# Performance work log

Hardware: AMD Instinct MI355X
Metric: run time of the kernel (lower is better)

The kernel has to match this reference:

```python
import jax, jax.numpy as jnp
import numpy as np

N_HEAD = 8
N_FEAT = 512
D_HEAD = N_FEAT // N_HEAD


def setup_inputs() -> dict:
    key = jax.random.key(0)
    ks = jax.random.split(key, 11)
    B, T, L = 4, 2048, 16
    s = 1.0 / np.sqrt(D_HEAD)
    so = 1.0 / np.sqrt(N_FEAT)
    return {
        "q": jax.random.normal(ks[0], (B, T, 1, N_FEAT), jnp.float32),
        "k": jax.random.normal(ks[1], (B, T, L, N_FEAT), jnp.float32),
        "v": jax.random.normal(ks[2], (B, T, L, N_FEAT), jnp.float32),
        "Wq": jax.random.uniform(ks[3], (D_HEAD, D_HEAD), jnp.float32, -s, s),
        "bq": jax.random.uniform(ks[4], (D_HEAD,), jnp.float32, -s, s),
        "Wk": jax.random.uniform(ks[5], (D_HEAD, D_HEAD), jnp.float32, -s, s),
        "bk": jax.random.uniform(ks[6], (D_HEAD,), jnp.float32, -s, s),
        "Wv": jax.random.uniform(ks[7], (D_HEAD, D_HEAD), jnp.float32, -s, s),
        "bv": jax.random.uniform(ks[8], (D_HEAD,), jnp.float32, -s, s),
        "Wo": jax.random.uniform(ks[9], (N_FEAT, N_FEAT), jnp.float32, -so, so),
        "bo": jax.random.uniform(ks[10], (N_FEAT,), jnp.float32, -so, so),
    }


def reference(q, k, v, Wq, bq, Wk, bk, Wv, bv, Wo, bo):
    B, T, L, F = k.shape
    H, D = N_HEAD, D_HEAD
    # split heads: q [B,T,H,D] (query axis of length 1 squeezed), k/v [B,T,L,H,D]
    qh = q.reshape(B, T, H, D)
    kh = k.reshape(B, T, L, H, D)
    vh = v.reshape(B, T, L, H, D)
    # per-head linear projections (shared across heads), Linear: x @ W^T + b
    qh = jnp.einsum("bthd,ed->bthe", qh, Wq) + bq
    kh = jnp.einsum("btlhd,ed->btlhe", kh, Wk) + bk
    vh = jnp.einsum("btlhd,ed->btlhe", vh, Wv) + bv
    # attention scores over the local window L (query length 1 per timestep)
    attw = jnp.einsum("bthd,btlhd->bthl", qh, kh) / jnp.sqrt(jnp.asarray(D, qh.dtype))
    attn = jax.nn.softmax(attw, axis=-1)  # dropout is identity in eval mode
    ct = jnp.einsum("bthl,btlhd->bthd", attn, vh)
    ct = ct.reshape(B, T, F)
    return ct @ Wo.T + bo
```

## Files before the change

### kernel.cpp

```cpp
#include <hip/hip_runtime.h>


#define NFEAT 512
#define NHEAD 8
#define DHEAD 64
#define LWIN  16
#define MPOS  16
#define LDSP  20

__device__ __forceinline__ float lanebcast(float x, int l) {
    return __uint_as_float(__builtin_amdgcn_readlane(__float_as_uint(x), l));
}

__global__ void precompute_small(const float* __restrict__ Wq, const float* __restrict__ bq,
                                 const float* __restrict__ Wk,
                                 const float* __restrict__ Wo, const float* __restrict__ bo,
                                 const float* __restrict__ bv,
                                 float* __restrict__ A, float* __restrict__ g,
                                 float* __restrict__ b2) {
    int idx = blockIdx.x * 256 + threadIdx.x;
    if (idx < 4096) {
        int d = idx >> 6, dp = idx & 63;
        float s = 0.f;
        #pragma unroll 8
        for (int e = 0; e < 64; ++e) s = fmaf(Wq[e * 64 + d], Wk[e * 64 + dp], s);
        A[idx] = s;
    } else if (idx < 4160) {
        int dp = idx - 4096;
        float s = 0.f;
        #pragma unroll 8
        for (int e = 0; e < 64; ++e) s = fmaf(Wk[e * 64 + dp], bq[e], s);
        g[dp] = s;
    } else if (idx < 4672) {
        int j = idx - 4160;
        float s = bo[j];
        #pragma unroll 8
        for (int i = 0; i < 512; ++i) s = fmaf(Wo[j * 512 + i], bv[i & 63], s);
        b2[j] = s;
    }
}

__global__ void precompute_wo2(const float* __restrict__ Wo, const float* __restrict__ Wv,
                               float* __restrict__ Wo2T) {
    int idx = blockIdx.x * 256 + threadIdx.x;
    int i = idx & 511, j = idx >> 9;
    int h = i >> 6, e = i & 63;
    float s = 0.f;
    #pragma unroll 8
    for (int d = 0; d < 64; ++d)
        s = fmaf(Wo[j * 512 + h * 64 + d], Wv[d * 64 + e], s);
    Wo2T[(size_t)i * 512 + j] = s;
}

__global__ __launch_bounds__(512, 4)
void attn_main(const float* __restrict__ q, const float* __restrict__ k,
               const float* __restrict__ v,
               const float* __restrict__ A, const float* __restrict__ g,
               const float* __restrict__ b2, const float* __restrict__ Wo2T,
               float* __restrict__ out) {
    __shared__ __align__(16) float vbarT[NFEAT * LDSP];

    const int tid  = threadIdx.x;
    const int lane = tid & 63;
    const int fe   = tid;
    const int bt0  = blockIdx.x * MPOS;

    float Areg[64];
    #pragma unroll
    for (int d = 0; d < 64; ++d) Areg[d] = A[d * 64 + lane];
    const float greg = g[lane];

    for (int p = 0; p < MPOS; ++p) {
        const int bt = bt0 + p;
        const float qv = q[(size_t)bt * NFEAT + fe];

        float w = greg;
        #pragma unroll
        for (int d = 0; d < 64; ++d)
            w = fmaf(lanebcast(qv, d), Areg[d], w);
        w *= 0.125f;

        const float* kp = k + (size_t)bt * (LWIN * NFEAT) + fe;
        float kv[LWIN];
        #pragma unroll
        for (int l = 0; l < LWIN; ++l) kv[l] = kp[(size_t)l * NFEAT];
        float sc[LWIN];
        #pragma unroll
        for (int l = 0; l < LWIN; ++l) sc[l] = w * kv[l];
        #pragma unroll
        for (int m = 1; m < 64; m <<= 1) {
            #pragma unroll
            for (int l = 0; l < LWIN; ++l) sc[l] += __shfl_xor(sc[l], m, 64);
        }

        float mx = sc[0];
        #pragma unroll
        for (int l = 1; l < LWIN; ++l) mx = fmaxf(mx, sc[l]);
        float sum = 0.f;
        #pragma unroll
        for (int l = 0; l < LWIN; ++l) { sc[l] = __expf(sc[l] - mx); sum += sc[l]; }
        const float inv = 1.0f / sum;

        const float* vp = v + (size_t)bt * (LWIN * NFEAT) + fe;
        float vb = 0.f;
        #pragma unroll
        for (int l = 0; l < LWIN; ++l) vb = fmaf(sc[l], vp[(size_t)l * NFEAT], vb);
        vbarT[fe * LDSP + p] = vb * inv;
    }
    __syncthreads();

    const int ph = tid >> 8;
    const int j0 = (tid & 255) * 2;

    float acc[8][2];
    #pragma unroll
    for (int pp = 0; pp < 8; ++pp) { acc[pp][0] = 0.f; acc[pp][1] = 0.f; }

    #pragma unroll 4
    for (int i = 0; i < NFEAT; ++i) {
        const float2 wo = *reinterpret_cast<const float2*>(&Wo2T[(size_t)i * 512 + j0]);
        const float4 va = *reinterpret_cast<const float4*>(&vbarT[i * LDSP + ph * 8]);
        const float4 vbq = *reinterpret_cast<const float4*>(&vbarT[i * LDSP + ph * 8 + 4]);
        const float vv0 = va.x, vv1 = va.y, vv2 = va.z, vv3 = va.w;
        const float vv4 = vbq.x, vv5 = vbq.y, vv6 = vbq.z, vv7 = vbq.w;
        acc[0][0] = fmaf(vv0, wo.x, acc[0][0]); acc[0][1] = fmaf(vv0, wo.y, acc[0][1]);
        acc[1][0] = fmaf(vv1, wo.x, acc[1][0]); acc[1][1] = fmaf(vv1, wo.y, acc[1][1]);
        acc[2][0] = fmaf(vv2, wo.x, acc[2][0]); acc[2][1] = fmaf(vv2, wo.y, acc[2][1]);
        acc[3][0] = fmaf(vv3, wo.x, acc[3][0]); acc[3][1] = fmaf(vv3, wo.y, acc[3][1]);
        acc[4][0] = fmaf(vv4, wo.x, acc[4][0]); acc[4][1] = fmaf(vv4, wo.y, acc[4][1]);
        acc[5][0] = fmaf(vv5, wo.x, acc[5][0]); acc[5][1] = fmaf(vv5, wo.y, acc[5][1]);
        acc[6][0] = fmaf(vv6, wo.x, acc[6][0]); acc[6][1] = fmaf(vv6, wo.y, acc[6][1]);
        acc[7][0] = fmaf(vv7, wo.x, acc[7][0]); acc[7][1] = fmaf(vv7, wo.y, acc[7][1]);
    }

    const float b20 = b2[j0], b21 = b2[j0 + 1];
    #pragma unroll
    for (int pp = 0; pp < 8; ++pp) {
        const int bt = bt0 + ph * 8 + pp;
        float2 o;
        o.x = acc[pp][0] + b20;
        o.y = acc[pp][1] + b21;
        *reinterpret_cast<float2*>(&out[(size_t)bt * NFEAT + j0]) = o;
    }
}

extern "C" void kernel_launch(void* const* d_in, const int* in_sizes, int n_in,
                              void* d_out, int out_size, void* d_ws, size_t ws_size,
                              hipStream_t stream) {
    const float* q  = (const float*)d_in[0];
    const float* k  = (const float*)d_in[1];
    const float* v  = (const float*)d_in[2];
    const float* Wq = (const float*)d_in[3];
    const float* bq = (const float*)d_in[4];
    const float* Wk = (const float*)d_in[5];
    const float* Wv = (const float*)d_in[7];
    const float* bv = (const float*)d_in[8];
    const float* Wo = (const float*)d_in[9];
    const float* bo = (const float*)d_in[10];
    float* out = (float*)d_out;

    float* ws   = (float*)d_ws;
    float* A    = ws;
    float* g    = ws + 4096;
    float* b2   = ws + 4160;
    float* Wo2T = ws + 4672;

    const int BT = in_sizes[0] / NFEAT;

    hipLaunchKernelGGL(precompute_small, dim3(19), dim3(256), 0, stream,
                       Wq, bq, Wk, Wo, bo, bv, A, g, b2);
    hipLaunchKernelGGL(precompute_wo2, dim3(1024), dim3(256), 0, stream,
                       Wo, Wv, Wo2T);
    hipLaunchKernelGGL(attn_main, dim3(BT / MPOS), dim3(512), 0, stream,
                       q, k, v, A, g, b2, Wo2T, out);
}
```

Before: 203.2 us.

## Split query-key projection into separate prepass kernel and halve positions per block

Moves the per-position q·A projection out of the main attention kernel into a new prepass kernel that stages A and q in LDS and writes the projected weights to workspace. The main kernel no longer holds 64 A values in registers, so launch bounds rise to 8 waves and each block covers 8 positions instead of 16, doubling the block count. The cost is an extra kernel launch and a global round trip for the Wm buffer, plus Wo2T being reread by twice as many blocks in the output projection.

```diff
diff --git a/kernel.cpp b/kernel.cpp
--- a/kernel.cpp
+++ b/kernel.cpp
@@ -5,12 +5,8 @@
 #define NHEAD 8
 #define DHEAD 64
 #define LWIN  16
-#define MPOS  16
-#define LDSP  20
-
-__device__ __forceinline__ float lanebcast(float x, int l) {
-    return __uint_as_float(__builtin_amdgcn_readlane(__float_as_uint(x), l));
-}
+#define MPOS  8
+#define LDSP  12
 
 __global__ void precompute_small(const float* __restrict__ Wq, const float* __restrict__ bq,
                                  const float* __restrict__ Wk,
@@ -52,41 +48,66 @@
     Wo2T[(size_t)i * 512 + j] = s;
 }
 
-__global__ __launch_bounds__(512, 4)
-void attn_main(const float* __restrict__ q, const float* __restrict__ k,
-               const float* __restrict__ v,
-               const float* __restrict__ A, const float* __restrict__ g,
-               const float* __restrict__ b2, const float* __restrict__ Wo2T,
-               float* __restrict__ out) {
+__global__ __launch_bounds__(512, 8)
+void w_prepass(const float* __restrict__ q, const float* __restrict__ A,
+               const float* __restrict__ g, float* __restrict__ Wm) {
+    __shared__ float As[4096];
+    __shared__ float qs[MPOS][NFEAT];
+    const int tid = threadIdx.x;
+    const int bt0 = blockIdx.x * MPOS;
+
+    #pragma unroll
+    for (int i = 0; i < 8; ++i) As[i * 512 + tid] = A[i * 512 + tid];
+    #pragma unroll
+    for (int r = 0; r < MPOS; ++r) qs[r][tid] = q[(size_t)(bt0 + r) * NFEAT + tid];
+    __syncthreads();
+
+    const int e  = tid & 63;
+    const int hb = (tid >> 6) << 6;
+    float acc[MPOS];
+    const float ge = g[e];
+    #pragma unroll
+    for (int r = 0; r < MPOS; ++r) acc[r] = ge;
+
+    #pragma unroll 4
+    for (int dq = 0; dq < 16; ++dq) {
+        const float a0 = As[(4 * dq + 0) * 64 + e];
+        const float a1 = As[(4 * dq + 1) * 64 + e];
+        const float a2 = As[(4 * dq + 2) * 64 + e];
+        const float a3 = As[(4 * dq + 3) * 64 + e];
+        #pragma unroll
+        for (int r = 0; r < MPOS; ++r) {
+            const float4 qv = *reinterpret_cast<const float4*>(&qs[r][hb + 4 * dq]);
+            acc[r] = fmaf(qv.x, a0, acc[r]);
+            acc[r] = fmaf(qv.y, a1, acc[r]);
+            acc[r] = fmaf(qv.z, a2, acc[r]);
+            acc[r] = fmaf(qv.w, a3, acc[r]);
+        }
+    }
+    #pragma unroll
+    for (int r = 0; r < MPOS; ++r)
+        Wm[(size_t)(bt0 + r) * NFEAT + tid] = acc[r] * 0.125f;
+}
+
+__global__ __launch_bounds__(512, 8)
+void attn_main(const float* __restrict__ Wm, const float* __restrict__ k,
+               const float* __restrict__ v, const float* __restrict__ b2,
+               const float* __restrict__ Wo2T, float* __restrict__ out) {
     __shared__ __align__(16) float vbarT[NFEAT * LDSP];
 
-    const int tid  = threadIdx.x;
-    const int lane = tid & 63;
-    const int fe   = tid;
-    const int bt0  = blockIdx.x * MPOS;
-
-    float Areg[64];
-    #pragma unroll
-    for (int d = 0; d < 64; ++d) Areg[d] = A[d * 64 + lane];
-    const float greg = g[lane];
+    const int tid = threadIdx.x;
+    const int fe  = tid;
+    const int bt0 = blockIdx.x * MPOS;
 
     for (int p = 0; p < MPOS; ++p) {
         const int bt = bt0 + p;
-        const float qv = q[(size_t)bt * NFEAT + fe];
+        const float wv = Wm[(size_t)bt * NFEAT + fe];
+        const float* kp = k + (size_t)bt * (LWIN * NFEAT) + fe;
+        const float* vp = v + (size_t)bt * (LWIN * NFEAT) + fe;
 
-        float w = greg;
-        #pragma unroll
-        for (int d = 0; d < 64; ++d)
-            w = fmaf(lanebcast(qv, d), Areg[d], w);
-        w *= 0.125f;
-
-        const float* kp = k + (size_t)bt * (LWIN * NFEAT) + fe;
-        float kv[LWIN];
-        #pragma unroll
-        for (int l = 0; l < LWIN; ++l) kv[l] = kp[(size_t)l * NFEAT];
         float sc[LWIN];
         #pragma unroll
-        for (int l = 0; l < LWIN; ++l) sc[l] = w * kv[l];
+        for (int l = 0; l < LWIN; ++l) sc[l] = wv * kp[(size_t)l * NFEAT];
         #pragma unroll
         for (int m = 1; m < 64; m <<= 1) {
             #pragma unroll
@@ -101,7 +122,6 @@
         for (int l = 0; l < LWIN; ++l) { sc[l] = __expf(sc[l] - mx); sum += sc[l]; }
         const float inv = 1.0f / sum;
 
-        const float* vp = v + (size_t)bt * (LWIN * NFEAT) + fe;
         float vb = 0.f;
         #pragma unroll
         for (int l = 0; l < LWIN; ++l) vb = fmaf(sc[l], vp[(size_t)l * NFEAT], vb);
@@ -112,31 +132,24 @@
     const int ph = tid >> 8;
     const int j0 = (tid & 255) * 2;
 
-    float acc[8][2];
+    float acc[4][2];
     #pragma unroll
-    for (int pp = 0; pp < 8; ++pp) { acc[pp][0] = 0.f; acc[pp][1] = 0.f; }
+    for (int pp = 0; pp < 4; ++pp) { acc[pp][0] = 0.f; acc[pp][1] = 0.f; }
 
     #pragma unroll 4
     for (int i = 0; i < NFEAT; ++i) {
         const float2 wo = *reinterpret_cast<const float2*>(&Wo2T[(size_t)i * 512 + j0]);
-        const float4 va = *reinterpret_cast<const float4*>(&vbarT[i * LDSP + ph * 8]);
-        const float4 vbq = *reinterpret_cast<const float4*>(&vbarT[i * LDSP + ph * 8 + 4]);
-        const float vv0 = va.x, vv1 = va.y, vv2 = va.z, vv3 = va.w;
-        const float vv4 = vbq.x, vv5 = vbq.y, vv6 = vbq.z, vv7 = vbq.w;
-        acc[0][0] = fmaf(vv0, wo.x, acc[0][0]); acc[0][1] = fmaf(vv0, wo.y, acc[0][1]);
-        acc[1][0] = fmaf(vv1, wo.x, acc[1][0]); acc[1][1] = fmaf(vv1, wo.y, acc[1][1]);
-        acc[2][0] = fmaf(vv2, wo.x, acc[2][0]); acc[2][1] = fmaf(vv2, wo.y, acc[2][1]);
-        acc[3][0] = fmaf(vv3, wo.x, acc[3][0]); acc[3][1] = fmaf(vv3, wo.y, acc[3][1]);
-        acc[4][0] = fmaf(vv4, wo.x, acc[4][0]); acc[4][1] = fmaf(vv4, wo.y, acc[4][1]);
-        acc[5][0] = fmaf(vv5, wo.x, acc[5][0]); acc[5][1] = fmaf(vv5, wo.y, acc[5][1]);
-        acc[6][0] = fmaf(vv6, wo.x, acc[6][0]); acc[6][1] = fmaf(vv6, wo.y, acc[6][1]);
-        acc[7][0] = fmaf(vv7, wo.x, acc[7][0]); acc[7][1] = fmaf(vv7, wo.y, acc[7][1]);
+        const float4 va = *reinterpret_cast<const float4*>(&vbarT[i * LDSP + ph * 4]);
+        acc[0][0] = fmaf(va.x, wo.x, acc[0][0]); acc[0][1] = fmaf(va.x, wo.y, acc[0][1]);
+        acc[1][0] = fmaf(va.y, wo.x, acc[1][0]); acc[1][1] = fmaf(va.y, wo.y, acc[1][1]);
+        acc[2][0] = fmaf(va.z, wo.x, acc[2][0]); acc[2][1] = fmaf(va.z, wo.y, acc[2][1]);
+        acc[3][0] = fmaf(va.w, wo.x, acc[3][0]); acc[3][1] = fmaf(va.w, wo.y, acc[3][1]);
     }
 
     const float b20 = b2[j0], b21 = b2[j0 + 1];
     #pragma unroll
-    for (int pp = 0; pp < 8; ++pp) {
-        const int bt = bt0 + ph * 8 + pp;
+    for (int pp = 0; pp < 4; ++pp) {
+        const int bt = bt0 + ph * 4 + pp;
         float2 o;
         o.x = acc[pp][0] + b20;
         o.y = acc[pp][1] + b21;
@@ -164,13 +177,16 @@
     float* g    = ws + 4096;
     float* b2   = ws + 4160;
     float* Wo2T = ws + 4672;
+    float* Wm   = ws + 4672 + 262144;
 
     const int BT = in_sizes[0] / NFEAT;
 
     hipLaunchKernelGGL(precompute_small, dim3(19), dim3(256), 0, stream,
                        Wq, bq, Wk, Wo, bo, bv, A, g, b2);
+    hipLaunchKernelGGL(w_prepass, dim3(BT / MPOS), dim3(512), 0, stream,
+                       q, A, g, Wm);
     hipLaunchKernelGGL(precompute_wo2, dim3(1024), dim3(256), 0, stream,
                        Wo, Wv, Wo2T);
     hipLaunchKernelGGL(attn_main, dim3(BT / MPOS), dim3(512), 0, stream,
-                       q, k, v, A, g, b2, Wo2T, out);
+                       Wm, k, v, b2, Wo2T, out);
 }
```

Measured after the change: 266.3 us. 31.0% more time.
